# Performance work log

Hardware: AMD Instinct MI355X
Metric: run time of the kernel (lower is better)

## Reference

```python
import jax, jax.numpy as jnp
from jax import lax
import numpy as np

DN = ('NCHW', 'OIHW', 'NCHW')

def conv2d(x, w, b, pad):
    y = lax.conv_general_dilated(x, w, (1, 1), [(pad, pad), (pad, pad)], dimension_numbers=DN)
    return y + b[None, :, None, None]

def setup_inputs() -> dict:
    key = jax.random.key(0)
    ks = jax.random.split(key, 20)
    B, C, H, W = 2, 256, 64, 64
    d = {}
    d['Fl'] = jax.random.normal(ks[0], (B, C, H, W), dtype=jnp.float32)
    d['Fv'] = jax.random.normal(ks[1], (B, C, H, W), dtype=jnp.float32)
    s3 = 1.0 / np.sqrt(C * 9)
    s1 = 1.0 / np.sqrt(C)
    names3 = ['Wqs', 'Wks', 'Wvs', 'Wqc', 'Wkc', 'Wvc']
    for i, n in enumerate(names3):
        d[n] = jax.random.normal(ks[2 + 2 * i], (C, C, 3, 3), dtype=jnp.float32) * s3
        d['b' + n[1:]] = jax.random.normal(ks[3 + 2 * i], (C,), dtype=jnp.float32) * 0.01
    d['Wgs'] = jax.random.normal(ks[14], (C, C, 1, 1), dtype=jnp.float32) * s1
    d['bgs'] = jax.random.normal(ks[15], (C,), dtype=jnp.float32) * 0.01
    d['Wfuse'] = jax.random.normal(ks[16], (C, 2 * C, 1, 1), dtype=jnp.float32) * (1.0 / np.sqrt(2 * C))
    d['bfuse'] = jax.random.normal(ks[17], (C,), dtype=jnp.float32) * 0.01
    return d

def reference(Fl, Fv, Wqs, bqs, Wks, bks, Wvs, bvs, Wqc, bqc, Wkc, bkc, Wvc, bvc, Wgs, bgs, Wfuse, bfuse):
    b, c, h, w = Fl.shape
    hw = h * w
    # --- self branch (on Fl) ---
    Qs = conv2d(Fl, Wqs, bqs, 1).reshape(b, c, hw)
    Ks = conv2d(Fl, Wks, bks, 1).reshape(b, c, hw)
    Vs = conv2d(Fl, Wvs, bvs, 1).reshape(b, c, hw)
    multi_s = jnp.einsum('bjk,bjq->bkq', Qs, Ks)          # [b, hw, hw]
    multi_s = jax.nn.softmax(multi_s, axis=1)              # softmax over dim=1 (as in torch code)
    Gs = jnp.einsum('bik,bjk->bij', multi_s, Vs)           # [b, hw, c]
    Gs = Gs.reshape(b, c, h, w)                            # raw reshape, faithful to torch
    Gs = conv2d(Gs, Wgs, bgs, 0) + Fl
    # --- cross branch (Q from Fl, K/V from Fv) ---
    Qc = conv2d(Fl, Wqc, bqc, 1).reshape(b, c, hw)
    Kc = conv2d(Fv, Wkc, bkc, 1).reshape(b, c, hw)
    Vc = conv2d(Fv, Wvc, bvc, 1).reshape(b, c, hw)
    multi_c = jnp.einsum('bjk,bjq->bkq', Qc, Kc)
    multi_c = jax.nn.softmax(multi_c, axis=1)
    Gc = jnp.einsum('bik,bjk->bij', multi_c, Vc)
    Gc = Gc.reshape(b, c, h, w)
    Gc = conv2d(Gc, Wgs, bgs, 0) + Fv                      # note: original uses Gs_conv for both branches
    out = conv2d(jnp.concatenate([Gs, Gc], axis=1), Wfuse, bfuse, 0)
    return out
```

## Files before the change

### kernel.cpp

```cpp
#include <hip/hip_runtime.h>

typedef __bf16 bf16x4 __attribute__((ext_vector_type(4)));
typedef __bf16 bf16x8 __attribute__((ext_vector_type(8)));
typedef float  f32x4  __attribute__((ext_vector_type(4)));

#define HWSZ 4096
#define CCH  256
#define LOG2E 1.44269504088896340736f

__device__ __forceinline__ float exp2_fast(float x) {
#if __has_builtin(__builtin_amdgcn_exp2f)
  return __builtin_amdgcn_exp2f(x);
#else
  return exp2f(x);
#endif
}

__device__ __forceinline__ void stage16(const __bf16* g, __bf16* ldsBase) {
#if __has_builtin(__builtin_amdgcn_global_load_lds)
  __builtin_amdgcn_global_load_lds(
      (const __attribute__((address_space(1))) void*)g,
      (__attribute__((address_space(3))) void*)ldsBase, 16, 0, 0);
#else
  int lane = threadIdx.x & 63;
  *(bf16x8*)(ldsBase + lane * 8) = *(const bf16x8*)g;
#endif
}

__global__ __launch_bounds__(256)
void gemm_conv(const __bf16* __restrict__ AL, const __bf16* __restrict__ AV,
               const __bf16* __restrict__ Cc,
               __bf16* __restrict__ qst, __bf16* __restrict__ kst,
               __bf16* __restrict__ vs,  __bf16* __restrict__ qct,
               __bf16* __restrict__ kct, __bf16* __restrict__ vc,
               const float* __restrict__ bqs, const float* __restrict__ bks,
               const float* __restrict__ bvs, const float* __restrict__ bqc,
               const float* __restrict__ bkc, const float* __restrict__ bvc)
{
  __shared__ __align__(16) __bf16 smem[8192];
  __bf16* As = smem;
  __bf16* Bs = smem + 4096;

  const int tid  = threadIdx.x;
  const int lane = tid & 63;
  const int w    = tid >> 6;
  const int wm   = (w >> 1) * 64;
  const int wn   = (w & 1) * 64;
  const int z    = blockIdx.z;
  const int by   = blockIdx.y;
  const int bn   = blockIdx.x * 128;
  const int K    = 2304;

  const bool isL = (by < 8);
  const int bm = (isL ? by : by - 8) * 128;
  const __bf16* Ab = isL ? AL : AV;
  const __bf16* Bb = Cc + (long)((isL ? 0 : 2) + z) * 9437184;

  f32x4 acc[4][4] = {};
  const int srow = lane >> 2;
  const int skc  = (lane & 3) * 8;

  for (int k0 = 0; k0 < K; k0 += 32) {
#pragma unroll
    for (int j = 0; j < 2; ++j) {
      int rbase = w * 32 + j * 16;
      stage16(Ab + (long)(bm + rbase + srow) * K + k0 + skc, As + rbase * 32);
    }
#pragma unroll
    for (int j = 0; j < 2; ++j) {
      int rbase = w * 32 + j * 16;
      stage16(Bb + (long)(bn + rbase + srow) * K + k0 + skc, Bs + rbase * 32);
    }
    __syncthreads();
    bf16x8 af[4], bfr[4];
#pragma unroll
    for (int t = 0; t < 4; ++t)
      af[t] = *(const bf16x8*)(As + (wm + t * 16 + (lane & 15)) * 32 + (lane >> 4) * 8);
#pragma unroll
    for (int t = 0; t < 4; ++t)
      bfr[t] = *(const bf16x8*)(Bs + (wn + t * 16 + (lane & 15)) * 32 + (lane >> 4) * 8);
#pragma unroll
    for (int mt = 0; mt < 4; ++mt)
#pragma unroll
      for (int nt = 0; nt < 4; ++nt)
        acc[mt][nt] = __builtin_amdgcn_mfma_f32_16x16x32_bf16(af[mt], bfr[nt], acc[mt][nt], 0, 0, 0);
    __syncthreads();
  }

#pragma unroll
  for (int mt = 0; mt < 4; ++mt) {
#pragma unroll
    for (int nt = 0; nt < 4; ++nt) {
#pragma unroll
      for (int r = 0; r < 4; ++r) {
        int m = bm + wm + mt * 16 + (lane >> 4) * 4 + r;
        int n = bn + wn + nt * 16 + (lane & 15);
        int g = m >> 8, mm = m & 255;
        const float* bias; __bf16* op; bool vlay;
        if (isL) {
          bias = (g == 0) ? bqs : (g == 1) ? bks : (g == 2) ? bvs : bqc;
          op   = (g == 0) ? qst : (g == 1) ? kst : (g == 2) ? vs  : qct;
          vlay = (g == 2);
        } else {
          bias = g ? bvc : bkc;
          op   = g ? vc  : kct;
          vlay = (g == 1);
        }
        float vv = acc[mt][nt][r] + bias[mm];
        if (vlay) op[(long)z * 1048576 + (long)mm * HWSZ + n] = (__bf16)vv;
        else      op[(long)z * 1048576 + (long)n * CCH + mm] = (__bf16)vv;
      }
    }
  }
}

__global__ __launch_bounds__(256)
void qk_stats(const __bf16* __restrict__ qs, const __bf16* __restrict__ qc,
              const __bf16* __restrict__ ks, const __bf16* __restrict__ kc,
              float* __restrict__ mst, float* __restrict__ lst)
{
  __shared__ __align__(16) __bf16 Kres[64 * 260];
  __shared__ float wm_[4][64], wl_[4][64];

  const int tid = threadIdx.x, lane = tid & 63, w = tid >> 6;
  const int quad = lane >> 4, l15 = lane & 15;
  const int lid = blockIdx.x;
  const int g = lid & 3;
  const int z = g & 1, br = g >> 1;
  const int qb = (lid >> 2) * 64;
  const __bf16* Qt = (br ? qc : qs) + (long)z * 1048576;
  const __bf16* Kt = (br ? kc : ks) + (long)z * 1048576;

  for (int idx = tid; idx < 2048; idx += 256) {
    int r = idx >> 5, c8 = (idx & 31) * 8;
    *(bf16x8*)(Kres + r * 260 + c8) = *(const bf16x8*)(Kt + (long)(qb + r) * 256 + c8);
  }
  __syncthreads();

  float rm[4], rl[4];
#pragma unroll
  for (int nt = 0; nt < 4; ++nt) { rm[nt] = -3.0e38f; rl[nt] = 0.f; }

  for (int it = 0; it < 16; ++it) {
    const int i0 = it * 256 + w * 64;
    f32x4 accS[4][4] = {};
#pragma unroll
    for (int cs = 0; cs < 256; cs += 32) {
      bf16x8 a[4], b[4];
#pragma unroll
      for (int mt = 0; mt < 4; ++mt)
        a[mt] = *(const bf16x8*)(Qt + (long)(i0 + mt * 16 + l15) * 256 + cs + quad * 8);
#pragma unroll
      for (int nt = 0; nt < 4; ++nt)
        b[nt] = *(const bf16x8*)(Kres + (nt * 16 + l15) * 260 + cs + quad * 8);
#pragma unroll
      for (int mt = 0; mt < 4; ++mt)
#pragma unroll
        for (int nt = 0; nt < 4; ++nt)
          accS[mt][nt] = __builtin_amdgcn_mfma_f32_16x16x32_bf16(a[mt], b[nt], accS[mt][nt], 0, 0, 0);
    }
#pragma unroll
    for (int nt = 0; nt < 4; ++nt) {
      float mx = -3.0e38f;
#pragma unroll
      for (int mt = 0; mt < 4; ++mt)
#pragma unroll
        for (int r = 0; r < 4; ++r) mx = fmaxf(mx, accS[mt][nt][r]);
      float sl = 0.f;
#pragma unroll
      for (int mt = 0; mt < 4; ++mt)
#pragma unroll
        for (int r = 0; r < 4; ++r) sl += exp2_fast((accS[mt][nt][r] - mx) * LOG2E);
#pragma unroll
      for (int d = 16; d <= 32; d <<= 1) {
        float om = __shfl_xor(mx, d, 64);
        float ol = __shfl_xor(sl, d, 64);
        float nm = fmaxf(mx, om);
        sl = sl * exp2_fast((mx - nm) * LOG2E) + ol * exp2_fast((om - nm) * LOG2E);
        mx = nm;
      }
      float nm = fmaxf(rm[nt], mx);
      rl[nt] = rl[nt] * exp2_fast((rm[nt] - nm) * LOG2E) + sl * exp2_fast((mx - nm) * LOG2E);
      rm[nt] = nm;
    }
  }
  if (lane < 16) {
#pragma unroll
    for (int nt = 0; nt < 4; ++nt) { wm_[w][nt * 16 + lane] = rm[nt]; wl_[w][nt * 16 + lane] = rl[nt]; }
  }
  __syncthreads();
  if (tid < 64) {
    float m = -3.0e38f;
#pragma unroll
    for (int ww = 0; ww < 4; ++ww) m = fmaxf(m, wm_[ww][tid]);
    float l = 0.f;
#pragma unroll
    for (int ww = 0; ww < 4; ++ww)
      l += wl_[ww][tid] * exp2_fast((wm_[ww][tid] - m) * LOG2E);
    long o = ((long)(br * 2 + z)) * 4096 + qb + tid;
    mst[o] = m;
    lst[o] = 1.0f / l;
  }
}

__global__ __launch_bounds__(256)
void fused_pv(const __bf16* __restrict__ qs, const __bf16* __restrict__ qc,
              const __bf16* __restrict__ ks, const __bf16* __restrict__ kc,
              const __bf16* __restrict__ vs, const __bf16* __restrict__ vc,
              const float* __restrict__ mst, const float* __restrict__ lst,
              float* __restrict__ gacc)
{
  __shared__ __align__(16) __bf16 Qres[64 * 260];
  __shared__ __align__(16) __bf16 Pl[64 * 132];
  __shared__ __align__(16) __bf16 Kst[128 * 32];

  const int tid = threadIdx.x, lane = tid & 63, w = tid >> 6;
  const int quad = lane >> 4, l15 = lane & 15;
  const int lid = blockIdx.x;
  const int g   = lid & 7;
  const int zbr = g >> 1;
  const int qh  = g & 1;
  const int bi  = (lid >> 3) * 64;
  const int br = zbr >> 1, z = zbr & 1;
  const __bf16* Qt = (br ? qc : qs) + (long)z * 1048576;
  const __bf16* Kt = (br ? kc : ks) + (long)z * 1048576;
  const __bf16* Vv = (br ? vc : vs) + (long)z * 1048576;
  const float* msp = mst + (long)zbr * 4096;
  const float* lsp = lst + (long)zbr * 4096;
  float* go = gacc + ((long)qh * 4 + zbr) * 1048576;

  for (int idx = tid; idx < 2048; idx += 256) {
    int r = idx >> 5, c8 = (idx & 31) * 8;
    *(bf16x8*)(Qres + r * 260 + c8) = *(const bf16x8*)(Qt + (long)(bi + r) * 256 + c8);
  }

  f32x4 accO[4][4] = {};
  const int srow = lane >> 2, skc = (lane & 3) * 8;
  const int q0 = qh * 2048;

  for (int qc0 = q0; qc0 < q0 + 2048; qc0 += 128) {
    f32x4 accS[4][2] = {};
#pragma unroll
    for (int cs = 0; cs < 256; cs += 32) {
#pragma unroll
      for (int jj = 0; jj < 2; ++jj) {
        int rbase = w * 32 + jj * 16;
        stage16(Kt + (long)(qc0 + rbase + srow) * 256 + cs + skc, Kst + rbase * 32);
      }
      __syncthreads();
      bf16x8 aq[4], bk[2];
#pragma unroll
      for (int mt = 0; mt < 4; ++mt)
        aq[mt] = *(const bf16x8*)(Qres + (mt * 16 + l15) * 260 + cs + quad * 8);
#pragma unroll
      for (int nt = 0; nt < 2; ++nt)
        bk[nt] = *(const bf16x8*)(Kst + (w * 32 + nt * 16 + l15) * 32 + quad * 8);
#pragma unroll
      for (int mt = 0; mt < 4; ++mt)
#pragma unroll
        for (int nt = 0; nt < 2; ++nt)
          accS[mt][nt] = __builtin_amdgcn_mfma_f32_16x16x32_bf16(aq[mt], bk[nt], accS[mt][nt], 0, 0, 0);
      __syncthreads();
    }
#pragma unroll
    for (int nt = 0; nt < 2; ++nt) {
      int q = w * 32 + nt * 16 + l15;
      float mq = msp[qc0 + q], lq = lsp[qc0 + q];
#pragma unroll
      for (int mt = 0; mt < 4; ++mt)
#pragma unroll
        for (int r = 0; r < 4; ++r) {
          int i = mt * 16 + quad * 4 + r;
          Pl[i * 132 + q] = (__bf16)(exp2_fast((accS[mt][nt][r] - mq) * LOG2E) * lq);
        }
    }
    __syncthreads();
#pragma unroll
    for (int qs0 = 0; qs0 < 128; qs0 += 32) {
      bf16x8 ap[4], bv[4];
#pragma unroll
      for (int mt = 0; mt < 4; ++mt)
        ap[mt] = *(const bf16x8*)(Pl + (mt * 16 + l15) * 132 + qs0 + quad * 8);
#pragma unroll
      for (int nt = 0; nt < 4; ++nt)
        bv[nt] = *(const bf16x8*)(Vv + (long)(w * 64 + nt * 16 + l15) * 4096 + qc0 + qs0 + quad * 8);
#pragma unroll
      for (int mt = 0; mt < 4; ++mt)
#pragma unroll
        for (int nt = 0; nt < 4; ++nt)
          accO[mt][nt] = __builtin_amdgcn_mfma_f32_16x16x32_bf16(ap[mt], bv[nt], accO[mt][nt], 0, 0, 0);
    }
  }
#pragma unroll
  for (int mt = 0; mt < 4; ++mt)
#pragma unroll
    for (int nt = 0; nt < 4; ++nt)
#pragma unroll
      for (int r = 0; r < 4; ++r) {
        int i = mt * 16 + quad * 4 + r;
        int j = w * 64 + nt * 16 + l15;
        go[(long)(bi + i) * 256 + j] = accO[mt][nt][r];
      }
}

__global__ __launch_bounds__(256)
void gsum_reshape(const float* __restrict__ ga, __bf16* __restrict__ gt) {
  __shared__ __bf16 lds[64 * 260];
  const int t = threadIdx.x, lane = t & 63, w = t >> 6;
  const int zbr = blockIdx.z;
  const int v   = blockIdx.y;
  const int jg  = blockIdx.x;
  const float* g0 = ga + (long)zbr * 1048576;
  const float* g1 = g0 + 4194304;
  for (int ci0 = 0; ci0 < 256; ci0 += 4) {
    int ci = ci0 + w;
    long src = (long)(ci * 16 + v) * 256 + jg * 64 + lane;
    lds[lane * 260 + ci] = (__bf16)(g0[src] + g1[src]);
  }
  __syncthreads();
  __bf16* out = gt + (long)zbr * 1048576 + ((long)v * 256 + jg * 64) * 256;
#pragma unroll
  for (int pp = 0; pp < 8; ++pp) {
    int idx = pp * 256 + t;
    int row = idx >> 5, c8 = (idx & 31) * 8;
    *(bf16x8*)(out + (long)row * 256 + c8) = *(const bf16x8*)(lds + row * 260 + c8);
  }
}

__global__ __launch_bounds__(256)
void wcomb(const float* __restrict__ Wgs, const float* __restrict__ bgs,
           const float* __restrict__ Wfu, const float* __restrict__ bfu,
           __bf16* __restrict__ WT, float* __restrict__ biasT)
{
  const int co = blockIdx.x, t = threadIdx.x;
  const float* wrow = Wfu + (long)co * 512;
  float accs = 0.f, accc = 0.f;
  for (int c = 0; c < 256; ++c) {
    float gv = Wgs[(long)c * 256 + t];
    accs = fmaf(wrow[c], gv, accs);
    accc = fmaf(wrow[c + 256], gv, accc);
  }
  __bf16* o = WT + (long)co * 1024;
  o[t]       = (__bf16)accs;
  o[256 + t] = (__bf16)accc;
  o[512 + t] = (__bf16)wrow[t];
  o[768 + t] = (__bf16)wrow[256 + t];
  __shared__ float red[256];
  red[t] = (wrow[t] + wrow[t + 256]) * bgs[t];
  __syncthreads();
  for (int s = 128; s > 0; s >>= 1) {
    if (t < s) red[t] += red[t + s];
    __syncthreads();
  }
  if (t == 0) biasT[co] = bfu[co] + red[0];
}

__global__ __launch_bounds__(256)
void tail_gemm(const __bf16* __restrict__ WT, const __bf16* __restrict__ GTS,
               const __bf16* __restrict__ Xt, const float* __restrict__ biasT,
               float* __restrict__ out)
{
  __shared__ __align__(16) __bf16 smem[8192];
  __bf16* As = smem;
  __bf16* Bs = smem + 4096;

  const int tid  = threadIdx.x;
  const int lane = tid & 63;
  const int w    = tid >> 6;
  const int wm   = (w >> 1) * 64;
  const int wn   = (w & 1) * 64;
  const int z    = blockIdx.z;
  const int bm   = blockIdx.y * 128;
  const int bn   = blockIdx.x * 128;

  const __bf16* Bsel[4] = {
    GTS + (long)z * 1048576, GTS + (long)(2 + z) * 1048576,
    Xt  + (long)z * 1048576, Xt  + (long)(2 + z) * 1048576
  };

  f32x4 acc[4][4] = {};
  const int srow = lane >> 2;
  const int skc  = (lane & 3) * 8;

  for (int k0 = 0; k0 < 1024; k0 += 32) {
    const __bf16* Bb = Bsel[k0 >> 8];
    const int kk = k0 & 255;
#pragma unroll
    for (int j = 0; j < 2; ++j) {
      int rbase = w * 32 + j * 16;
      stage16(WT + (long)(bm + rbase + srow) * 1024 + k0 + skc, As + rbase * 32);
    }
#pragma unroll
    for (int j = 0; j < 2; ++j) {
      int rbase = w * 32 + j * 16;
      stage16(Bb + (long)(bn + rbase + srow) * 256 + kk + skc, Bs + rbase * 32);
    }
    __syncthreads();
    bf16x8 af[4], bfr[4];
#pragma unroll
    for (int t = 0; t < 4; ++t)
      af[t] = *(const bf16x8*)(As + (wm + t * 16 + (lane & 15)) * 32 + (lane >> 4) * 8);
#pragma unroll
    for (int t = 0; t < 4; ++t)
      bfr[t] = *(const bf16x8*)(Bs + (wn + t * 16 + (lane & 15)) * 32 + (lane >> 4) * 8);
#pragma unroll
    for (int mt = 0; mt < 4; ++mt)
#pragma unroll
      for (int nt = 0; nt < 4; ++nt)
        acc[mt][nt] = __builtin_amdgcn_mfma_f32_16x16x32_bf16(af[mt], bfr[nt], acc[mt][nt], 0, 0, 0);
    __syncthreads();
  }

#pragma unroll
  for (int mt = 0; mt < 4; ++mt)
#pragma unroll
    for (int nt = 0; nt < 4; ++nt)
#pragma unroll
      for (int r = 0; r < 4; ++r) {
        int m = bm + wm + mt * 16 + (lane >> 4) * 4 + r;
        int n = bn + wn + nt * 16 + (lane & 15);
        out[((long)z * 256 + m) * HWSZ + n] = acc[mt][nt][r] + biasT[m];
      }
}

__global__ void transpose_cvt(const float* __restrict__ F0, const float* __restrict__ F1,
                              __bf16* __restrict__ Xt) {
  __shared__ float tile[32][33];
  int img = blockIdx.z;
  const float* src = (img < 2 ? F0 : F1) + (long)(img & 1) * (CCH * HWSZ);
  __bf16* dst = Xt + (long)img * (HWSZ * CCH);
  int p0 = blockIdx.x * 32, c0 = blockIdx.y * 32;
  int tx = threadIdx.x, ty = threadIdx.y;
#pragma unroll
  for (int j = 0; j < 32; j += 8)
    tile[ty + j][tx] = src[(long)(c0 + ty + j) * HWSZ + p0 + tx];
  __syncthreads();
#pragma unroll
  for (int j = 0; j < 32; j += 8)
    dst[(long)(p0 + ty + j) * CCH + c0 + tx] = (__bf16)tile[tx][ty + j];
}

__global__ void im2col_k(const __bf16* __restrict__ Xt, __bf16* __restrict__ Cc) {
  int img = blockIdx.y;
  int e = blockIdx.x * 256 + threadIdx.x;
  int p = e / 288;
  int c8 = e - p * 288;
  int t = c8 >> 5;
  int ci0 = (c8 & 31) * 8;
  int dy = t / 3 - 1, dx = t - (t / 3) * 3 - 1;
  int y = p >> 6, x = p & 63;
  int yy = y + dy, xx = x + dx;
  const __bf16* src = Xt + (long)img * (HWSZ * CCH);
  __bf16* dst = Cc + (long)img * 9437184 + (long)p * 2304 + t * 256 + ci0;
  uint4 v = make_uint4(0u, 0u, 0u, 0u);
  if ((unsigned)yy < 64u && (unsigned)xx < 64u)
    v = *(const uint4*)(src + (long)(yy * 64 + xx) * CCH + ci0);
  *(uint4*)dst = v;
}

struct W6 { const float* w[6]; };
__global__ void repack_w3(W6 wp, __bf16* __restrict__ AL, __bf16* __restrict__ AV) {
  int zi = blockIdx.y;
  int e = blockIdx.x * 256 + threadIdx.x;
  int co = e / 2304;
  int rem = e - co * 2304;
  int t = rem >> 8, ci = rem & 255;
  float v = wp.w[zi][(long)co * 2304 + ci * 9 + t];
  __bf16* dst = (zi < 4) ? (AL + (long)zi * 256 * 2304) : (AV + (long)(zi - 4) * 256 * 2304);
  dst[(long)co * 2304 + rem] = (__bf16)v;
}

extern "C" void kernel_launch(void* const* d_in, const int* in_sizes, int n_in,
                              void* d_out, int out_size, void* d_ws, size_t ws_size,
                              hipStream_t stream) {
  const float* Fl  = (const float*)d_in[0];
  const float* Fv  = (const float*)d_in[1];
  const float* Wqs = (const float*)d_in[2];  const float* bqs = (const float*)d_in[3];
  const float* Wks = (const float*)d_in[4];  const float* bks = (const float*)d_in[5];
  const float* Wvs = (const float*)d_in[6];  const float* bvs = (const float*)d_in[7];
  const float* Wqc = (const float*)d_in[8];  const float* bqc = (const float*)d_in[9];
  const float* Wkc = (const float*)d_in[10]; const float* bkc = (const float*)d_in[11];
  const float* Wvc = (const float*)d_in[12]; const float* bvc = (const float*)d_in[13];
  const float* Wgs = (const float*)d_in[14]; const float* bgs = (const float*)d_in[15];
  const float* Wfu = (const float*)d_in[16]; const float* bfu = (const float*)d_in[17];

  char* ws = (char*)d_ws;
  size_t off = 0;
  auto take = [&](size_t bytes) -> void* {
    void* p = ws + off; off = (off + bytes + 255) & ~(size_t)255; return p;
  };
  __bf16* QST  = (__bf16*)take(4194304);
  __bf16* KST  = (__bf16*)take(4194304);
  __bf16* QCT  = (__bf16*)take(4194304);
  __bf16* KCT  = (__bf16*)take(4194304);
  __bf16* VS   = (__bf16*)take(4194304);
  __bf16* VC   = (__bf16*)take(4194304);
  __bf16* GTS  = (__bf16*)take(8388608);
  __bf16* AL   = (__bf16*)take(4718592);
  __bf16* AV   = (__bf16*)take(2359296);
  __bf16* WT   = (__bf16*)take(524288);
  float*  BT   = (float*)take(1024);
  float*  MST  = (float*)take(65536);
  float*  LST  = (float*)take(65536);
  __bf16* Xt   = (__bf16*)take(8388608);
  size_t ovl = off;
  __bf16* Cc = (__bf16*)take(75497472);
  size_t needConv = off;
  float* GACC = (float*)(ws + ovl);
  size_t needAttn = ovl + 33554432;
  size_t need = needConv > needAttn ? needConv : needAttn;
  if (ws_size < need) return;

  transpose_cvt<<<dim3(128, 8, 4), dim3(32, 8), 0, stream>>>(Fl, Fv, Xt);
  im2col_k<<<dim3(4608, 4), 256, 0, stream>>>(Xt, Cc);
  W6 wp; wp.w[0]=Wqs; wp.w[1]=Wks; wp.w[2]=Wvs; wp.w[3]=Wqc; wp.w[4]=Wkc; wp.w[5]=Wvc;
  repack_w3<<<dim3(2304, 6), 256, 0, stream>>>(wp, AL, AV);
  wcomb<<<dim3(256), 256, 0, stream>>>(Wgs, bgs, Wfu, bfu, WT, BT);

  gemm_conv<<<dim3(32, 12, 2), 256, 0, stream>>>(
      AL, AV, Cc, QST, KST, VS, QCT, KCT, VC,
      bqs, bks, bvs, bqc, bkc, bvc);

  qk_stats<<<dim3(256), 256, 0, stream>>>(QST, QCT, KST, KCT, MST, LST);

  fused_pv<<<dim3(512), 256, 0, stream>>>(
      QST, QCT, KST, KCT, VS, VC, MST, LST, GACC);

  gsum_reshape<<<dim3(4, 16, 4), 256, 0, stream>>>(GACC, GTS);

  tail_gemm<<<dim3(32, 2, 2), 256, 0, stream>>>(WT, GTS, Xt, BT, (float*)d_out);
}
```

Measured before the change: 467.4 us.

## Keep Q fragments in registers and double-buffer K staging in fused_pv

In fused_pv, each wave now holds its own 16 Q rows as MFMA A-fragments in registers instead of staging a 64x256 Q tile in shared memory, and computes S for all 128 key columns. The K chunk staging is double-buffered so the next 32-channel chunk is loaded while MFMAs run on the current one, which also drops one barrier per chunk. This cuts LDS footprint and LDS read traffic for Q, at the cost of more VGPRs (8 bf16x8 Q fragments plus 8 accumulators) and a changed wave-to-tile mapping.

```diff
diff --git a/kernel.cpp b/kernel.cpp
--- a/kernel.cpp
+++ b/kernel.cpp
@@ -210,9 +210,8 @@
               const float* __restrict__ mst, const float* __restrict__ lst,
               float* __restrict__ gacc)
 {
-  __shared__ __align__(16) __bf16 Qres[64 * 260];
+  __shared__ __align__(16) __bf16 Kst[2][128 * 32];
   __shared__ __align__(16) __bf16 Pl[64 * 132];
-  __shared__ __align__(16) __bf16 Kst[128 * 32];
 
   const int tid = threadIdx.x, lane = tid & 63, w = tid >> 6;
   const int quad = lane >> 4, l15 = lane & 15;
@@ -229,50 +228,51 @@
   const float* lsp = lst + (long)zbr * 4096;
   float* go = gacc + ((long)qh * 4 + zbr) * 1048576;
 
-  for (int idx = tid; idx < 2048; idx += 256) {
-    int r = idx >> 5, c8 = (idx & 31) * 8;
-    *(bf16x8*)(Qres + r * 260 + c8) = *(const bf16x8*)(Qt + (long)(bi + r) * 256 + c8);
-  }
+  bf16x8 aqr[8];
+#pragma unroll
+  for (int c8 = 0; c8 < 8; ++c8)
+    aqr[c8] = *(const bf16x8*)(Qt + (long)(bi + w * 16 + l15) * 256 + c8 * 32 + quad * 8);
 
   f32x4 accO[4][4] = {};
   const int srow = lane >> 2, skc = (lane & 3) * 8;
   const int q0 = qh * 2048;
 
-  for (int qc0 = q0; qc0 < q0 + 2048; qc0 += 128) {
-    f32x4 accS[4][2] = {};
-#pragma unroll
-    for (int cs = 0; cs < 256; cs += 32) {
-#pragma unroll
-      for (int jj = 0; jj < 2; ++jj) {
-        int rbase = w * 32 + jj * 16;
-        stage16(Kt + (long)(qc0 + rbase + srow) * 256 + cs + skc, Kst + rbase * 32);
+  for (int qt = 0; qt < 16; ++qt) {
+    const int qc0 = q0 + qt * 128;
+#pragma unroll
+    for (int jj = 0; jj < 2; ++jj) {
+      int rbase = w * 32 + jj * 16;
+      stage16(Kt + (long)(qc0 + rbase + srow) * 256 + skc, Kst[0] + rbase * 32);
+    }
+    __syncthreads();
+    f32x4 accS[8] = {};
+#pragma unroll
+    for (int cs = 0; cs < 8; ++cs) {
+      if (cs < 7) {
+#pragma unroll
+        for (int jj = 0; jj < 2; ++jj) {
+          int rbase = w * 32 + jj * 16;
+          stage16(Kt + (long)(qc0 + rbase + srow) * 256 + (cs + 1) * 32 + skc,
+                  Kst[(cs + 1) & 1] + rbase * 32);
+        }
+      }
+      const __bf16* kb = Kst[cs & 1];
+#pragma unroll
+      for (int nt = 0; nt < 8; ++nt) {
+        bf16x8 bk = *(const bf16x8*)(kb + (nt * 16 + l15) * 32 + quad * 8);
+        accS[nt] = __builtin_amdgcn_mfma_f32_16x16x32_bf16(aqr[cs], bk, accS[nt], 0, 0, 0);
       }
       __syncthreads();
-      bf16x8 aq[4], bk[2];
-#pragma unroll
-      for (int mt = 0; mt < 4; ++mt)
-        aq[mt] = *(const bf16x8*)(Qres + (mt * 16 + l15) * 260 + cs + quad * 8);
-#pragma unroll
-      for (int nt = 0; nt < 2; ++nt)
-        bk[nt] = *(const bf16x8*)(Kst + (w * 32 + nt * 16 + l15) * 32 + quad * 8);
-#pragma unroll
-      for (int mt = 0; mt < 4; ++mt)
-#pragma unroll
-        for (int nt = 0; nt < 2; ++nt)
-          accS[mt][nt] = __builtin_amdgcn_mfma_f32_16x16x32_bf16(aq[mt], bk[nt], accS[mt][nt], 0, 0, 0);
-      __syncthreads();
-    }
-#pragma unroll
-    for (int nt = 0; nt < 2; ++nt) {
-      int q = w * 32 + nt * 16 + l15;
+    }
+#pragma unroll
+    for (int nt = 0; nt < 8; ++nt) {
+      int q = nt * 16 + l15;
       float mq = msp[qc0 + q], lq = lsp[qc0 + q];
 #pragma unroll
-      for (int mt = 0; mt < 4; ++mt)
-#pragma unroll
-        for (int r = 0; r < 4; ++r) {
-          int i = mt * 16 + quad * 4 + r;
-          Pl[i * 132 + q] = (__bf16)(exp2_fast((accS[mt][nt][r] - mq) * LOG2E) * lq);
-        }
+      for (int r = 0; r < 4; ++r) {
+        int i = w * 16 + quad * 4 + r;
+        Pl[i * 132 + q] = (__bf16)(exp2_fast((accS[nt][r] - mq) * LOG2E) * lq);
+      }
     }
     __syncthreads();
 #pragma unroll
```

After: 467.1 us. About the same (-0.1%).

## Swizzle LDS tiles in GEMMs and split softmax stats over two blocks

Applied to the files above, without the earlier changes.

Applies an XOR swizzle to the 16-byte chunk offsets used when staging and reading 32-wide LDS tiles in gemm_conv, fused_pv and tail_gemm, to reduce LDS bank conflicts on the MFMA operand reads. Separately, qk_stats now splits the softmax-normalisation reduction over the i dimension across two blocks (512 instead of 256 blocks). A new stats_combine2 kernel merges the partial max and sum values. This raises occupancy on the large GPU at the cost of an extra launch and a small scratch buffer.

```diff
diff --git a/kernel.cpp b/kernel.cpp
--- a/kernel.cpp
+++ b/kernel.cpp
@@ -26,6 +26,9 @@
   *(bf16x8*)(ldsBase + lane * 8) = *(const bf16x8*)g;
 #endif
 }
+
+#define SWZ_STAGE(lane) ((((lane) & 3) ^ (((lane) >> 3) & 3)) * 8)
+#define SWZ_READ(quad, lane) ((((quad) ^ (((lane) >> 1) & 3))) * 8)
 
 __global__ __launch_bounds__(256)
 void gemm_conv(const __bf16* __restrict__ AL, const __bf16* __restrict__ AV,
@@ -58,7 +61,9 @@
 
   f32x4 acc[4][4] = {};
   const int srow = lane >> 2;
-  const int skc  = (lane & 3) * 8;
+  const int skc  = SWZ_STAGE(lane);
+  const int quad = lane >> 4, l15 = lane & 15;
+  const int rdo  = SWZ_READ(quad, lane);
 
   for (int k0 = 0; k0 < K; k0 += 32) {
 #pragma unroll
@@ -75,10 +80,10 @@
     bf16x8 af[4], bfr[4];
 #pragma unroll
     for (int t = 0; t < 4; ++t)
-      af[t] = *(const bf16x8*)(As + (wm + t * 16 + (lane & 15)) * 32 + (lane >> 4) * 8);
+      af[t] = *(const bf16x8*)(As + (wm + t * 16 + l15) * 32 + rdo);
 #pragma unroll
     for (int t = 0; t < 4; ++t)
-      bfr[t] = *(const bf16x8*)(Bs + (wn + t * 16 + (lane & 15)) * 32 + (lane >> 4) * 8);
+      bfr[t] = *(const bf16x8*)(Bs + (wn + t * 16 + l15) * 32 + rdo);
 #pragma unroll
     for (int mt = 0; mt < 4; ++mt)
 #pragma unroll
@@ -93,8 +98,8 @@
     for (int nt = 0; nt < 4; ++nt) {
 #pragma unroll
       for (int r = 0; r < 4; ++r) {
-        int m = bm + wm + mt * 16 + (lane >> 4) * 4 + r;
-        int n = bn + wn + nt * 16 + (lane & 15);
+        int m = bm + wm + mt * 16 + quad * 4 + r;
+        int n = bn + wn + nt * 16 + l15;
         int g = m >> 8, mm = m & 255;
         const float* bias; __bf16* op; bool vlay;
         if (isL) {
@@ -117,7 +122,7 @@
 __global__ __launch_bounds__(256)
 void qk_stats(const __bf16* __restrict__ qs, const __bf16* __restrict__ qc,
               const __bf16* __restrict__ ks, const __bf16* __restrict__ kc,
-              float* __restrict__ mst, float* __restrict__ lst)
+              float* __restrict__ pm, float* __restrict__ pl)
 {
   __shared__ __align__(16) __bf16 Kres[64 * 260];
   __shared__ float wm_[4][64], wl_[4][64];
@@ -127,7 +132,8 @@
   const int lid = blockIdx.x;
   const int g = lid & 3;
   const int z = g & 1, br = g >> 1;
-  const int qb = (lid >> 2) * 64;
+  const int ih = (lid >> 2) & 1;
+  const int qb = (lid >> 3) * 64;
   const __bf16* Qt = (br ? qc : qs) + (long)z * 1048576;
   const __bf16* Kt = (br ? kc : ks) + (long)z * 1048576;
 
@@ -141,8 +147,8 @@
 #pragma unroll
   for (int nt = 0; nt < 4; ++nt) { rm[nt] = -3.0e38f; rl[nt] = 0.f; }
 
-  for (int it = 0; it < 16; ++it) {
-    const int i0 = it * 256 + w * 64;
+  for (int it = 0; it < 8; ++it) {
+    const int i0 = ih * 2048 + it * 256 + w * 64;
     f32x4 accS[4][4] = {};
 #pragma unroll
     for (int cs = 0; cs < 256; cs += 32) {
@@ -197,10 +203,22 @@
 #pragma unroll
     for (int ww = 0; ww < 4; ++ww)
       l += wl_[ww][tid] * exp2_fast((wm_[ww][tid] - m) * LOG2E);
-    long o = ((long)(br * 2 + z)) * 4096 + qb + tid;
-    mst[o] = m;
-    lst[o] = 1.0f / l;
-  }
+    long o = ((long)ih * 4 + br * 2 + z) * 4096 + qb + tid;
+    pm[o] = m;
+    pl[o] = l;
+  }
+}
+
+__global__ void stats_combine2(const float* __restrict__ pm, const float* __restrict__ pl,
+                               float* __restrict__ mst, float* __restrict__ lst) {
+  int q = blockIdx.x * 256 + threadIdx.x;
+  int zbr = blockIdx.y;
+  float m0 = pm[(long)zbr * 4096 + q],        l0 = pl[(long)zbr * 4096 + q];
+  float m1 = pm[(long)(4 + zbr) * 4096 + q],  l1 = pl[(long)(4 + zbr) * 4096 + q];
+  float m = fmaxf(m0, m1);
+  float l = l0 * exp2_fast((m0 - m) * LOG2E) + l1 * exp2_fast((m1 - m) * LOG2E);
+  mst[(long)zbr * 4096 + q] = m;
+  lst[(long)zbr * 4096 + q] = 1.0f / l;
 }
 
 __global__ __launch_bounds__(256)
@@ -235,7 +253,9 @@
   }
 
   f32x4 accO[4][4] = {};
-  const int srow = lane >> 2, skc = (lane & 3) * 8;
+  const int srow = lane >> 2;
+  const int skc  = SWZ_STAGE(lane);
+  const int rdo  = SWZ_READ(quad, lane);
   const int q0 = qh * 2048;
 
   for (int qc0 = q0; qc0 < q0 + 2048; qc0 += 128) {
@@ -254,7 +274,7 @@
         aq[mt] = *(const bf16x8*)(Qres + (mt * 16 + l15) * 260 + cs + quad * 8);
 #pragma unroll
       for (int nt = 0; nt < 2; ++nt)
-        bk[nt] = *(const bf16x8*)(Kst + (w * 32 + nt * 16 + l15) * 32 + quad * 8);
+        bk[nt] = *(const bf16x8*)(Kst + (w * 32 + nt * 16 + l15) * 32 + rdo);
 #pragma unroll
       for (int mt = 0; mt < 4; ++mt)
 #pragma unroll
@@ -380,7 +400,9 @@
 
   f32x4 acc[4][4] = {};
   const int srow = lane >> 2;
-  const int skc  = (lane & 3) * 8;
+  const int skc  = SWZ_STAGE(lane);
+  const int quad = lane >> 4, l15 = lane & 15;
+  const int rdo  = SWZ_READ(quad, lane);
 
   for (int k0 = 0; k0 < 1024; k0 += 32) {
     const __bf16* Bb = Bsel[k0 >> 8];
@@ -399,10 +421,10 @@
     bf16x8 af[4], bfr[4];
 #pragma unroll
     for (int t = 0; t < 4; ++t)
-      af[t] = *(const bf16x8*)(As + (wm + t * 16 + (lane & 15)) * 32 + (lane >> 4) * 8);
+      af[t] = *(const bf16x8*)(As + (wm + t * 16 + l15) * 32 + rdo);
 #pragma unroll
     for (int t = 0; t < 4; ++t)
-      bfr[t] = *(const bf16x8*)(Bs + (wn + t * 16 + (lane & 15)) * 32 + (lane >> 4) * 8);
+      bfr[t] = *(const bf16x8*)(Bs + (wn + t * 16 + l15) * 32 + rdo);
 #pragma unroll
     for (int mt = 0; mt < 4; ++mt)
 #pragma unroll
@@ -417,8 +439,8 @@
     for (int nt = 0; nt < 4; ++nt)
 #pragma unroll
       for (int r = 0; r < 4; ++r) {
-        int m = bm + wm + mt * 16 + (lane >> 4) * 4 + r;
-        int n = bn + wn + nt * 16 + (lane & 15);
+        int m = bm + wm + mt * 16 + quad * 4 + r;
+        int n = bn + wn + nt * 16 + l15;
         out[((long)z * 256 + m) * HWSZ + n] = acc[mt][nt][r] + biasT[m];
       }
 }
@@ -502,6 +524,8 @@
   float*  BT   = (float*)take(1024);
   float*  MST  = (float*)take(65536);
   float*  LST  = (float*)take(65536);
+  float*  PM   = (float*)take(131072);
+  float*  PL   = (float*)take(131072);
   __bf16* Xt   = (__bf16*)take(8388608);
   size_t ovl = off;
   __bf16* Cc = (__bf16*)take(75497472);
@@ -521,7 +545,8 @@
       AL, AV, Cc, QST, KST, VS, QCT, KCT, VC,
       bqs, bks, bvs, bqc, bkc, bvc);
 
-  qk_stats<<<dim3(256), 256, 0, stream>>>(QST, QCT, KST, KCT, MST, LST);
+  qk_stats<<<dim3(512), 256, 0, stream>>>(QST, QCT, KST, KCT, PM, PL);
+  stats_combine2<<<dim3(16, 4), 256, 0, stream>>>(PM, PL, MST, LST);
 
   fused_pv<<<dim3(512), 256, 0, stream>>>(
       QST, QCT, KST, KCT, VS, VC, MST, LST, GACC);
```

After: 443.6 us. -5.1%, faster.
